# Kernel tuning notes

Hardware: AMD Instinct MI355X
Metric: run time of the kernel (lower is better)

## Reference

```python
import jax, jax.numpy as jnp
import numpy as np

FEATURE_MAPS = (38, 19, 10, 5, 3, 1)
BOXES_PER_LOC = (4, 6, 6, 6, 4, 4)
IMAGE_SIZE = 300
DEC_SIZE = 64  # WhatDecoder output resolution
MAX_OBJECTS = 10
Z_WHAT = 64


def _recon_indices():
    # Maps per-prior slots (8732) to per-location slots (1940), matching
    # Decoder.reconstruction_indices: each location index repeated boxes_per_loc times.
    idx, last = [], 0
    for fm, bpl in zip(FEATURE_MAPS, BOXES_PER_LOC):
        loc = np.arange(fm * fm) + last
        idx.append(np.repeat(loc, bpl))
        last = loc[-1] + 1
    return jnp.asarray(np.concatenate(idx), dtype=jnp.int32)


def _deconv2x2(x, W, b):
    # ConvTranspose2d(kernel=2, stride=2): each input pixel expands to a 2x2 block.
    n, c, h, w = x.shape
    o = W.shape[1]
    y = jnp.einsum('nchw,coab->nohawb', x, W).reshape(n, o, 2 * h, 2 * w)
    return y + b[None, :, None, None]


def _what_decoder(z, params):
    # z (M, Z_WHAT) -> (M, 3, 64, 64) in [0,1]
    x = z[:, :, None, None]
    nl = len(params)
    for i, (W, b) in enumerate(params):
        x = _deconv2x2(x, W, b)
        x = jax.nn.relu(x) if i < nl - 1 else jax.nn.sigmoid(x)
    return x


def _stn(images, z_where):
    # Spatial transformer: place (M,3,S,S) glyphs into IMAGE_SIZE canvas at box
    # z_where (M,4) = (cx,cy,w,h) in [0,1]; bilinear sampling, zeros padding.
    M, _, S, _ = images.shape
    cx, cy, w, h = (z_where[:, i] for i in range(4))
    # output pixel centers in normalized [-1,1] coords (align_corners=False)
    coords = (2.0 * jnp.arange(IMAGE_SIZE, dtype=images.dtype) + 1.0) / IMAGE_SIZE - 1.0
    xo = coords[None, None, :]
    yo = coords[None, :, None]
    eps = 1e-6
    u = (xo - (2.0 * cx - 1.0)[:, None, None]) / (w[:, None, None] + eps)  # (M,H,W)
    v = (yo - (2.0 * cy - 1.0)[:, None, None]) / (h[:, None, None] + eps)
    ix = ((u + 1.0) * S - 1.0) / 2.0  # input pixel coords
    iy = ((v + 1.0) * S - 1.0) / 2.0

    def sample_one(img, iy, ix):
        iy0 = jnp.floor(iy)
        ix0 = jnp.floor(ix)
        wy1 = iy - iy0
        wx1 = ix - ix0
        wy0 = 1.0 - wy1
        wx0 = 1.0 - wx1

        def g(y, x):
            yi = jnp.clip(y, 0, S - 1).astype(jnp.int32)
            xi = jnp.clip(x, 0, S - 1).astype(jnp.int32)
            valid = ((y >= 0) & (y < S) & (x >= 0) & (x < S)).astype(img.dtype)
            return img[:, yi, xi] * valid  # (3,H,W)

        return (g(iy0, ix0) * wy0 * wx0 + g(iy0, ix0 + 1) * wy0 * wx1
                + g(iy0 + 1, ix0) * wy1 * wx0 + g(iy0 + 1, ix0 + 1) * wy1 * wx1)

    return jax.vmap(sample_one)(images, iy, ix)  # (M,3,H,H)


def setup_inputs() -> dict:
    key = jax.random.key(0)
    ks = jax.random.split(key, 20)
    B, NLOC, NPRI = 16, 1940, 8732
    chans = (Z_WHAT, 256, 128, 64, 32, 16, 3)
    inp = {
        'z_what': jax.random.normal(ks[0], (B, NLOC, Z_WHAT), jnp.float32),
        'z_where': jax.random.uniform(ks[1], (B, NPRI, 4), jnp.float32),
        'z_present': jax.random.randint(ks[2], (B, NPRI, 1), 0, 2, jnp.int32),
        'z_depth': jax.random.normal(ks[3], (B, NLOC, 1), jnp.float32),
    }
    for i in range(6):
        ci, co = chans[i], chans[i + 1]
        inp[f'W{i}'] = jax.random.normal(ks[4 + i], (ci, co, 2, 2), jnp.float32) * 0.1
        inp[f'b{i}'] = jnp.zeros((co,), jnp.float32)
    return inp


def reference(z_what, z_where, z_present, z_depth,
              W0, b0, W1, b1, W2, b2, W3, b3, W4, b4, W5, b5):
    params = [(W0, b0), (W1, b1), (W2, b2), (W3, b3), (W4, b4), (W5, b5)]
    idx = _recon_indices()
    zw = z_what[:, idx]      # (B, P, D) ragged location->prior gather
    zd = z_depth[:, idx, 0]  # (B, P)
    order = jnp.argsort(-zd, axis=1)[:, :MAX_OBJECTS]  # depth sort, descending
    B, K = order.shape

    def gat(t):
        return jnp.take_along_axis(
            t, jnp.broadcast_to(order[:, :, None], (B, K, t.shape[-1])), axis=1)

    sw = gat(zw)            # (B,K,D)
    swr = gat(z_where)      # (B,K,4)
    sp = gat(z_present)     # (B,K,1)

    decoded = _what_decoder(sw.reshape(B * K, Z_WHAT), params)      # (B*K,3,64,64)
    transformed = _stn(decoded, swr.reshape(B * K, 4))              # (B*K,3,300,300)
    present = (sp == 1).astype(transformed.dtype).reshape(B * K, 1, 1, 1)
    objs = (transformed * present).reshape(B, K, 3, IMAGE_SIZE, IMAGE_SIZE)

    # z-buffer merge: per pixel, take first nonzero object in depth order
    nz = objs != 0.0
    first = nz & (jnp.cumsum(nz.astype(jnp.int32), axis=1) == 1)
    return jnp.sum(objs * first.astype(objs.dtype), axis=1)  # (B,3,300,300)
```

## Files before the change

### kernel.cpp

```cpp
#include <hip/hip_runtime.h>
#include <cmath>

#define NLOC 1940
#define NPRI 8732
#define BATCH 16
#define KOBJ 10

__device__ __forceinline__ int loc_of_prior(int p) {
    if (p < 5776) return p >> 2;
    if (p < 7942) return 1444 + (p - 5776) / 6;
    if (p < 8542) return 1805 + (p - 7942) / 6;
    if (p < 8692) return 1905 + (p - 8542) / 6;
    if (p < 8728) return 1930 + ((p - 8692) >> 2);
    return 1939 + ((p - 8728) >> 2);
}

__global__ __launch_bounds__(256) void topk_kernel(
    const float* __restrict__ z_what, const float* __restrict__ z_where,
    const int* __restrict__ z_present, const float* __restrict__ z_depth,
    float* __restrict__ gathered, float* __restrict__ paramsF, int* __restrict__ paramsI)
{
    const int b = blockIdx.x, tid = threadIdx.x;
    __shared__ float zd[NPRI];
    __shared__ float rv[256];
    __shared__ int   ri[256];
    __shared__ int   ord[KOBJ];
    __shared__ int   locs[KOBJ];

    for (int p = tid; p < NPRI; p += 256) zd[p] = z_depth[b * NLOC + loc_of_prior(p)];
    __syncthreads();

    for (int k = 0; k < KOBJ; ++k) {
        float bv = -INFINITY; int bi = NPRI;
        for (int p = tid; p < NPRI; p += 256) {
            float v = zd[p];
            if (v > bv) { bv = v; bi = p; }
        }
        rv[tid] = bv; ri[tid] = bi;
        __syncthreads();
        for (int s = 128; s > 0; s >>= 1) {
            if (tid < s) {
                float v2 = rv[tid + s]; int i2 = ri[tid + s];
                if (v2 > rv[tid] || (v2 == rv[tid] && i2 < ri[tid])) { rv[tid] = v2; ri[tid] = i2; }
            }
            __syncthreads();
        }
        if (tid == 0) {
            int w = ri[0];
            ord[k] = w; locs[k] = loc_of_prior(w);
            zd[w] = -INFINITY;
        }
        __syncthreads();
    }

    for (int e = tid; e < KOBJ * 64; e += 256) {
        int k = e >> 6, c = e & 63;
        gathered[(b * KOBJ + k) * 64 + c] = z_what[(b * NLOC + locs[k]) * 64 + c];
    }

    if (tid == 0) {
        int cnt = 0;
        for (int k = 0; k < KOBJ; ++k) {
            int p = ord[k];
            if (z_present[b * NPRI + p] == 1) {
                const float* zw = z_where + (b * NPRI + p) * 4;
                float cx = zw[0], cy = zw[1], w_ = zw[2], h_ = zw[3];
                float* pf = paramsF + (b * KOBJ + cnt) * 4;
                pf[0] = __fadd_rn(w_, 1e-6f);
                pf[1] = __fadd_rn(h_, 1e-6f);
                pf[2] = __fsub_rn(__fmul_rn(2.0f, cx), 1.0f);
                pf[3] = __fsub_rn(__fmul_rn(2.0f, cy), 1.0f);
                paramsI[b * 12 + 2 + cnt] = b * KOBJ + k;
                cnt++;
            }
        }
        paramsI[b * 12] = cnt;
    }
}

__global__ __launch_bounds__(256) void repack_kernel(
    const float* __restrict__ W0, const float* __restrict__ W1, float* __restrict__ Wr)
{
    const int idx = blockIdx.x * 256 + threadIdx.x;
    if (idx < 65536) {
        int q = idx >> 14, rem = idx & 16383, c = rem >> 8, o = rem & 255;
        Wr[idx] = W0[(((c << 8) | o) << 2) + q];
    } else {
        int i2 = idx - 65536;
        int q = i2 >> 15, rem = i2 & 32767, c = rem >> 7, o = rem & 127;
        Wr[idx] = W1[(((c << 7) | o) << 2) + q];
    }
}

__global__ __launch_bounds__(256) void dec_fused(
    const float* __restrict__ gathered, const float* __restrict__ Wr,
    const float* __restrict__ b0v, const float* __restrict__ b1v,
    const float* __restrict__ W2, const float* __restrict__ b2v,
    const float* __restrict__ W3, const float* __restrict__ b3v,
    const float* __restrict__ W4, const float* __restrict__ b4v,
    const float* __restrict__ W5, const float* __restrict__ b5v,
    float* __restrict__ decoded)
{
    __shared__ __align__(16) float P[4096];
    __shared__ __align__(16) float Q[2048];
    __shared__ __align__(16) float Zs[256];
    const int r  = blockIdx.x;
    const int g  = blockIdx.y;
    const int t  = threadIdx.x;
    const int y1 = r >> 2, x1 = r & 3;
    const int q0 = (y1 >> 1) * 2 + (x1 >> 1);
    const int p1 = (y1 & 1) * 2 + (x1 & 1);
    const int s4 = g * 4;

    Zs[t] = gathered[(s4 + (t & 3)) * 64 + (t >> 2)];
    __syncthreads();

    {
        const float* w0 = Wr + q0 * 16384 + t;
        float bv = b0v[t];
        float4 acc = make_float4(bv, bv, bv, bv);
        #pragma unroll 8
        for (int c = 0; c < 64; ++c) {
            float w = w0[c << 8];
            float4 xs = *reinterpret_cast<const float4*>(Zs + (c << 2));
            acc.x = fmaf(xs.x, w, acc.x); acc.y = fmaf(xs.y, w, acc.y);
            acc.z = fmaf(xs.z, w, acc.z); acc.w = fmaf(xs.w, w, acc.w);
        }
        float4 rv = make_float4(fmaxf(acc.x, 0.f), fmaxf(acc.y, 0.f),
                                fmaxf(acc.z, 0.f), fmaxf(acc.w, 0.f));
        *reinterpret_cast<float4*>(P + (t << 2)) = rv;
    }
    __syncthreads();

    {
        const int o = t & 127, h = t >> 7;
        const float* w1 = Wr + 65536 + p1 * 32768 + o;
        float4 acc;
        if (h == 0) { float bv = b1v[o]; acc = make_float4(bv, bv, bv, bv); }
        else        { acc = make_float4(0.f, 0.f, 0.f, 0.f); }
        const int cb = h << 7;
        #pragma unroll 8
        for (int c = 0; c < 128; ++c) {
            float w = w1[(cb + c) << 7];
            float4 xs = *reinterpret_cast<const float4*>(P + ((cb + c) << 2));
            acc.x = fmaf(xs.x, w, acc.x); acc.y = fmaf(xs.y, w, acc.y);
            acc.z = fmaf(xs.z, w, acc.z); acc.w = fmaf(xs.w, w, acc.w);
        }
        if (h == 1) *reinterpret_cast<float4*>(P + 1024 + (o << 2)) = acc;
        __syncthreads();
        if (h == 0) {
            float4 p2 = *reinterpret_cast<const float4*>(P + 1024 + (o << 2));
            acc.x += p2.x; acc.y += p2.y; acc.z += p2.z; acc.w += p2.w;
            float4 rv = make_float4(fmaxf(acc.x, 0.f), fmaxf(acc.y, 0.f),
                                    fmaxf(acc.z, 0.f), fmaxf(acc.w, 0.f));
            *reinterpret_cast<float4*>(Q + (o << 2)) = rv;
        }
    }
    __syncthreads();

    {
        const float* w2 = W2 + t;
        float bv = b2v[t >> 2];
        float4 acc = make_float4(bv, bv, bv, bv);
        #pragma unroll 8
        for (int ci = 0; ci < 128; ++ci) {
            float w = w2[ci << 8];
            float4 xs = *reinterpret_cast<const float4*>(Q + (ci << 2));
            acc.x = fmaf(xs.x, w, acc.x); acc.y = fmaf(xs.y, w, acc.y);
            acc.z = fmaf(xs.z, w, acc.z); acc.w = fmaf(xs.w, w, acc.w);
        }
        float4 rv = make_float4(fmaxf(acc.x, 0.f), fmaxf(acc.y, 0.f),
                                fmaxf(acc.z, 0.f), fmaxf(acc.w, 0.f));
        *reinterpret_cast<float4*>(P + (t << 2)) = rv;
    }
    __syncthreads();

    {
        const int px = t & 15, coa = t >> 4;
        const int ly = px >> 2, lx = px & 3;
        const int par = (ly >> 1) * 2 + (lx >> 1);
        const int wp  = (ly & 1) * 2 + (lx & 1);
        const float* w3 = W3 + coa * 4 + wp;
        float bva = b3v[coa], bvb = b3v[coa + 16];
        float4 a0 = make_float4(bva, bva, bva, bva);
        float4 a1 = make_float4(bvb, bvb, bvb, bvb);
        #pragma unroll 4
        for (int ci = 0; ci < 64; ++ci) {
            float4 xs = *reinterpret_cast<const float4*>(P + (ci << 4) + (par << 2));
            float wa = w3[ci << 7];
            float wb = w3[(ci << 7) + 64];
            a0.x = fmaf(xs.x, wa, a0.x); a0.y = fmaf(xs.y, wa, a0.y);
            a0.z = fmaf(xs.z, wa, a0.z); a0.w = fmaf(xs.w, wa, a0.w);
            a1.x = fmaf(xs.x, wb, a1.x); a1.y = fmaf(xs.y, wb, a1.y);
            a1.z = fmaf(xs.z, wb, a1.z); a1.w = fmaf(xs.w, wb, a1.w);
        }
        float4 r0 = make_float4(fmaxf(a0.x, 0.f), fmaxf(a0.y, 0.f),
                                fmaxf(a0.z, 0.f), fmaxf(a0.w, 0.f));
        float4 r1 = make_float4(fmaxf(a1.x, 0.f), fmaxf(a1.y, 0.f),
                                fmaxf(a1.z, 0.f), fmaxf(a1.w, 0.f));
        *reinterpret_cast<float4*>(Q + (coa << 6) + (px << 2)) = r0;
        *reinterpret_cast<float4*>(Q + ((coa + 16) << 6) + (px << 2)) = r1;
    }
    __syncthreads();

    {
        const int px = t & 63, co0 = t >> 6;
        const int ly = px >> 3, lx = px & 7;
        const int par = (ly >> 1) * 4 + (lx >> 1);
        const int wp  = (ly & 1) * 2 + (lx & 1);
        const float* w4 = W4 + co0 * 4 + wp;
        float4 acc[4];
        #pragma unroll
        for (int k = 0; k < 4; ++k) {
            float bv = b4v[co0 + 4 * k];
            acc[k] = make_float4(bv, bv, bv, bv);
        }
        #pragma unroll 4
        for (int ci = 0; ci < 32; ++ci) {
            float4 xs = *reinterpret_cast<const float4*>(Q + (ci << 6) + (par << 2));
            #pragma unroll
            for (int k = 0; k < 4; ++k) {
                float w = w4[(ci << 6) + k * 16];
                acc[k].x = fmaf(xs.x, w, acc[k].x); acc[k].y = fmaf(xs.y, w, acc[k].y);
                acc[k].z = fmaf(xs.z, w, acc[k].z); acc[k].w = fmaf(xs.w, w, acc[k].w);
            }
        }
        #pragma unroll
        for (int k = 0; k < 4; ++k) {
            float4 rv = make_float4(fmaxf(acc[k].x, 0.f), fmaxf(acc[k].y, 0.f),
                                    fmaxf(acc[k].z, 0.f), fmaxf(acc[k].w, 0.f));
            *reinterpret_cast<float4*>(P + ((co0 + 4 * k) << 8) + (px << 2)) = rv;
        }
    }
    __syncthreads();

    {
        const int px = t;
        const int ly = px >> 4, lx = px & 15;
        const int par = (ly >> 1) * 8 + (lx >> 1);
        const int wp  = (ly & 1) * 2 + (lx & 1);
        const int gy = y1 * 16 + ly, gx = x1 * 16 + lx;
        const float* w5 = W5 + wp;
        float4 acc[3];
        #pragma unroll
        for (int c = 0; c < 3; ++c) {
            float bv = b5v[c];
            acc[c] = make_float4(bv, bv, bv, bv);
        }
        #pragma unroll 4
        for (int ci = 0; ci < 16; ++ci) {
            float4 xs = *reinterpret_cast<const float4*>(P + (ci << 8) + (par << 2));
            #pragma unroll
            for (int c = 0; c < 3; ++c) {
                float w = w5[ci * 12 + c * 4];
                acc[c].x = fmaf(xs.x, w, acc[c].x); acc[c].y = fmaf(xs.y, w, acc[c].y);
                acc[c].z = fmaf(xs.z, w, acc[c].z); acc[c].w = fmaf(xs.w, w, acc[c].w);
            }
        }
        const int pbase = (gy * 64 + gx) * 3;
        #pragma unroll
        for (int c = 0; c < 3; ++c) {
            float vs[4] = {acc[c].x, acc[c].y, acc[c].z, acc[c].w};
            #pragma unroll
            for (int s = 0; s < 4; ++s)
                decoded[(s4 + s) * 12288 + pbase + c] = 1.0f / (1.0f + expf(-vs[s]));
        }
    }
}

__global__ __launch_bounds__(256) void stn_kernel(
    const float* __restrict__ decoded, const float* __restrict__ paramsF,
    const int* __restrict__ paramsI, float* __restrict__ out)
{
    const int b = blockIdx.y;
    __shared__ float sp[KOBJ][4];
    __shared__ int ssamp[KOBJ];
    __shared__ int scnt;
    if (threadIdx.x == 0) scnt = paramsI[b * 12];
    if (threadIdx.x < KOBJ) {
        #pragma unroll
        for (int c = 0; c < 4; ++c) sp[threadIdx.x][c] = paramsF[(b * KOBJ + threadIdx.x) * 4 + c];
        ssamp[threadIdx.x] = paramsI[b * 12 + 2 + threadIdx.x];
    }
    __syncthreads();
    const int pix = blockIdx.x * 256 + threadIdx.x;
    if (pix >= 90000) return;
    const int y = pix / 300;
    const int x = pix - y * 300;
    const float xo = __fsub_rn(__fdiv_rn(__fadd_rn(__fmul_rn(2.0f, (float)x), 1.0f), 300.0f), 1.0f);
    const float yo = __fsub_rn(__fdiv_rn(__fadd_rn(__fmul_rn(2.0f, (float)y), 1.0f), 300.0f), 1.0f);

    float o0 = 0.0f, o1 = 0.0f, o2 = 0.0f;
    bool d0 = false, d1 = false, d2 = false;
    const int cnt = scnt;
    for (int k = 0; k < cnt; ++k) {
        const float u = __fdiv_rn(__fsub_rn(xo, sp[k][2]), sp[k][0]);
        const float v = __fdiv_rn(__fsub_rn(yo, sp[k][3]), sp[k][1]);
        const float ix = __fmul_rn(__fsub_rn(__fmul_rn(__fadd_rn(u, 1.0f), 64.0f), 1.0f), 0.5f);
        const float iy = __fmul_rn(__fsub_rn(__fmul_rn(__fadd_rn(v, 1.0f), 64.0f), 1.0f), 0.5f);
        if (!(ix > -1.0f && ix < 64.0f && iy > -1.0f && iy < 64.0f)) continue;

        const float ix0f = floorf(ix), iy0f = floorf(iy);
        const float ix1f = __fadd_rn(ix0f, 1.0f), iy1f = __fadd_rn(iy0f, 1.0f);
        const float wx1 = __fsub_rn(ix, ix0f), wy1 = __fsub_rn(iy, iy0f);
        const float wx0 = __fsub_rn(1.0f, wx1), wy0 = __fsub_rn(1.0f, wy1);
        const bool vx0 = (ix0f >= 0.0f) && (ix0f < 64.0f);
        const bool vx1 = (ix1f >= 0.0f) && (ix1f < 64.0f);
        const bool vy0 = (iy0f >= 0.0f) && (iy0f < 64.0f);
        const bool vy1 = (iy1f >= 0.0f) && (iy1f < 64.0f);
        const int x0  = (int)fminf(fmaxf(ix0f, 0.0f), 63.0f);
        const int x1  = (int)fminf(fmaxf(ix1f, 0.0f), 63.0f);
        const int y0i = (int)fminf(fmaxf(iy0f, 0.0f), 63.0f);
        const int y1i = (int)fminf(fmaxf(iy1f, 0.0f), 63.0f);
        const int r00 = y0i * 64 + x0, r01 = y0i * 64 + x1;
        const int r10 = y1i * 64 + x0, r11 = y1i * 64 + x1;
        const bool m00 = vy0 && vx0, m01 = vy0 && vx1, m10 = vy1 && vx0, m11 = vy1 && vx1;
        const float* img = decoded + ssamp[k] * 12288;

        float g00x = 0.f, g00y = 0.f, g00z = 0.f;
        float g01x = 0.f, g01y = 0.f, g01z = 0.f;
        float g10x = 0.f, g10y = 0.f, g10z = 0.f;
        float g11x = 0.f, g11y = 0.f, g11z = 0.f;
        if (m00) { const float* p = img + r00 * 3; g00x = p[0]; g00y = p[1]; g00z = p[2]; }
        if (m01) { const float* p = img + r01 * 3; g01x = p[0]; g01y = p[1]; g01z = p[2]; }
        if (m10) { const float* p = img + r10 * 3; g10x = p[0]; g10y = p[1]; g10z = p[2]; }
        if (m11) { const float* p = img + r11 * 3; g11x = p[0]; g11y = p[1]; g11z = p[2]; }

        if (!d0) {
            float val = g00x * wy0 * wx0 + g01x * wy0 * wx1 + g10x * wy1 * wx0 + g11x * wy1 * wx1;
            if (val != 0.0f) { o0 = val; d0 = true; }
        }
        if (!d1) {
            float val = g00y * wy0 * wx0 + g01y * wy0 * wx1 + g10y * wy1 * wx0 + g11y * wy1 * wx1;
            if (val != 0.0f) { o1 = val; d1 = true; }
        }
        if (!d2) {
            float val = g00z * wy0 * wx0 + g01z * wy0 * wx1 + g10z * wy1 * wx0 + g11z * wy1 * wx1;
            if (val != 0.0f) { o2 = val; d2 = true; }
        }
        if (d0 && d1 && d2) break;
    }
    const int ob = b * 270000 + pix;
    out[ob] = o0;
    out[ob + 90000] = o1;
    out[ob + 180000] = o2;
}

extern "C" void kernel_launch(void* const* d_in, const int* in_sizes, int n_in,
                              void* d_out, int out_size, void* d_ws, size_t ws_size,
                              hipStream_t stream)
{
    const float* z_what    = (const float*)d_in[0];
    const float* z_where   = (const float*)d_in[1];
    const int*   z_present = (const int*)d_in[2];
    const float* z_depth   = (const float*)d_in[3];
    const float* W0 = (const float*)d_in[4];   const float* b0 = (const float*)d_in[5];
    const float* W1 = (const float*)d_in[6];   const float* b1 = (const float*)d_in[7];
    const float* W2 = (const float*)d_in[8];   const float* b2 = (const float*)d_in[9];
    const float* W3 = (const float*)d_in[10];  const float* b3 = (const float*)d_in[11];
    const float* W4 = (const float*)d_in[12];  const float* b4 = (const float*)d_in[13];
    const float* W5 = (const float*)d_in[14];  const float* b5 = (const float*)d_in[15];

    float* ws = (float*)d_ws;
    float* gathered = ws;
    float* paramsF  = ws + 16384;
    int*   paramsI  = (int*)(ws + 17408);
    float* decoded  = ws + 32768;
    float* Wr       = (float*)d_out;
    float* outp     = (float*)d_out;

    hipLaunchKernelGGL(repack_kernel, dim3(768), dim3(256), 0, stream, W0, W1, Wr);
    hipLaunchKernelGGL(topk_kernel, dim3(BATCH), dim3(256), 0, stream,
                       z_what, z_where, z_present, z_depth, gathered, paramsF, paramsI);
    hipLaunchKernelGGL(dec_fused, dim3(16, 40), dim3(256), 0, stream,
                       gathered, Wr, b0, b1, W2, b2, W3, b3, W4, b4, W5, b5, decoded);
    hipLaunchKernelGGL(stn_kernel, dim3(352, BATCH), dim3(256), 0, stream,
                       decoded, paramsF, paramsI, outp);
}
```

Measured before the change: 165.6 us.

## Top-3 over locations, decode only unique glyphs, fuse prep, hoist STN row math

The top-10 over 8732 repeated priors is replaced with a top-3 over the 1940 unique locations, since each location expands to at least four consecutive priors. Only three distinct glyphs per batch are decoded instead of ten (decoder grid shrinks from 40 to 12 in y). The weight repack and the top-k are merged into one launch. The STN kernel precomputes per-row vertical sampling terms in shared memory and skips objects that do not cover the block's rows. This relies on tie-break equivalence between the prior ordering and the location ordering, and adds some shared-memory setup per STN block.

```diff
diff --git a/kernel.cpp b/kernel.cpp
--- a/kernel.cpp
+++ b/kernel.cpp
@@ -6,89 +6,96 @@
 #define BATCH 16
 #define KOBJ 10
 
-__device__ __forceinline__ int loc_of_prior(int p) {
-    if (p < 5776) return p >> 2;
-    if (p < 7942) return 1444 + (p - 5776) / 6;
-    if (p < 8542) return 1805 + (p - 7942) / 6;
-    if (p < 8692) return 1905 + (p - 8542) / 6;
-    if (p < 8728) return 1930 + ((p - 8692) >> 2);
-    return 1939 + ((p - 8728) >> 2);
+__device__ __forceinline__ void ins3(float v, int i,
+    float& a0, float& a1, float& a2, int& j0, int& j1, int& j2)
+{
+    if (v > a0 || (v == a0 && i < j0)) { a2=a1; j2=j1; a1=a0; j1=j0; a0=v; j0=i; }
+    else if (v > a1 || (v == a1 && i < j1)) { a2=a1; j2=j1; a1=v; j1=i; }
+    else if (v > a2 || (v == a2 && i < j2)) { a2=v; j2=i; }
 }
 
-__global__ __launch_bounds__(256) void topk_kernel(
+__global__ __launch_bounds__(256) void prep_kernel(
+    const float* __restrict__ W0, const float* __restrict__ W1, float* __restrict__ Wr,
     const float* __restrict__ z_what, const float* __restrict__ z_where,
     const int* __restrict__ z_present, const float* __restrict__ z_depth,
     float* __restrict__ gathered, float* __restrict__ paramsF, int* __restrict__ paramsI)
 {
-    const int b = blockIdx.x, tid = threadIdx.x;
-    __shared__ float zd[NPRI];
-    __shared__ float rv[256];
-    __shared__ int   ri[256];
-    __shared__ int   ord[KOBJ];
-    __shared__ int   locs[KOBJ];
-
-    for (int p = tid; p < NPRI; p += 256) zd[p] = z_depth[b * NLOC + loc_of_prior(p)];
-    __syncthreads();
-
-    for (int k = 0; k < KOBJ; ++k) {
-        float bv = -INFINITY; int bi = NPRI;
-        for (int p = tid; p < NPRI; p += 256) {
-            float v = zd[p];
-            if (v > bv) { bv = v; bi = p; }
-        }
-        rv[tid] = bv; ri[tid] = bi;
+    __shared__ float sv[768];
+    __shared__ int   si[768];
+    __shared__ int   locs3[3];
+    const int tid = threadIdx.x;
+
+    if (blockIdx.x < 768) {
+        const int idx = blockIdx.x * 256 + tid;
+        if (idx < 65536) {
+            int q = idx >> 14, rem = idx & 16383, c = rem >> 8, o = rem & 255;
+            Wr[idx] = W0[(((c << 8) | o) << 2) + q];
+        } else {
+            int i2 = idx - 65536;
+            int q = i2 >> 15, rem = i2 & 32767, c = rem >> 7, o = rem & 127;
+            Wr[idx] = W1[(((c << 7) | o) << 2) + q];
+        }
+        return;
+    }
+
+    const int b = blockIdx.x - 768;
+    float v0 = -INFINITY, v1 = -INFINITY, v2 = -INFINITY;
+    int   i0 = NLOC, i1 = NLOC, i2 = NLOC;
+    for (int i = tid; i < NLOC; i += 256) {
+        float v = z_depth[b * NLOC + i];
+        ins3(v, i, v0, v1, v2, i0, i1, i2);
+    }
+    sv[tid*3+0] = v0; sv[tid*3+1] = v1; sv[tid*3+2] = v2;
+    si[tid*3+0] = i0; si[tid*3+1] = i1; si[tid*3+2] = i2;
+    __syncthreads();
+    for (int s = 128; s > 0; s >>= 1) {
+        if (tid < s) {
+            float a0 = sv[tid*3], a1 = sv[tid*3+1], a2 = sv[tid*3+2];
+            int   j0 = si[tid*3], j1 = si[tid*3+1], j2 = si[tid*3+2];
+            const int o = tid + s;
+            ins3(sv[o*3+0], si[o*3+0], a0, a1, a2, j0, j1, j2);
+            ins3(sv[o*3+1], si[o*3+1], a0, a1, a2, j0, j1, j2);
+            ins3(sv[o*3+2], si[o*3+2], a0, a1, a2, j0, j1, j2);
+            sv[tid*3] = a0; sv[tid*3+1] = a1; sv[tid*3+2] = a2;
+            si[tid*3] = j0; si[tid*3+1] = j1; si[tid*3+2] = j2;
+        }
         __syncthreads();
-        for (int s = 128; s > 0; s >>= 1) {
-            if (tid < s) {
-                float v2 = rv[tid + s]; int i2 = ri[tid + s];
-                if (v2 > rv[tid] || (v2 == rv[tid] && i2 < ri[tid])) { rv[tid] = v2; ri[tid] = i2; }
-            }
-            __syncthreads();
-        }
-        if (tid == 0) {
-            int w = ri[0];
-            ord[k] = w; locs[k] = loc_of_prior(w);
-            zd[w] = -INFINITY;
-        }
-        __syncthreads();
-    }
-
-    for (int e = tid; e < KOBJ * 64; e += 256) {
-        int k = e >> 6, c = e & 63;
-        gathered[(b * KOBJ + k) * 64 + c] = z_what[(b * NLOC + locs[k]) * 64 + c];
     }
 
     if (tid == 0) {
-        int cnt = 0;
-        for (int k = 0; k < KOBJ; ++k) {
-            int p = ord[k];
-            if (z_present[b * NPRI + p] == 1) {
-                const float* zw = z_where + (b * NPRI + p) * 4;
-                float cx = zw[0], cy = zw[1], w_ = zw[2], h_ = zw[3];
-                float* pf = paramsF + (b * KOBJ + cnt) * 4;
-                pf[0] = __fadd_rn(w_, 1e-6f);
-                pf[1] = __fadd_rn(h_, 1e-6f);
-                pf[2] = __fsub_rn(__fmul_rn(2.0f, cx), 1.0f);
-                pf[3] = __fsub_rn(__fmul_rn(2.0f, cy), 1.0f);
-                paramsI[b * 12 + 2 + cnt] = b * KOBJ + k;
-                cnt++;
+        int cnt = 0, taken = 0;
+        for (int j = 0; j < 3; ++j) {
+            int L = si[j];
+            locs3[j] = L;
+            if (taken >= KOBJ) continue;
+            int start, bpl;
+            if (L < 1444)      { start = 4 * L;                 bpl = 4; }
+            else if (L < 1805) { start = 5776 + 6 * (L - 1444); bpl = 6; }
+            else if (L < 1905) { start = 7942 + 6 * (L - 1805); bpl = 6; }
+            else if (L < 1930) { start = 8542 + 6 * (L - 1905); bpl = 6; }
+            else if (L < 1939) { start = 8692 + 4 * (L - 1930); bpl = 4; }
+            else               { start = 8728;                  bpl = 4; }
+            for (int o = 0; o < bpl && taken < KOBJ; ++o, ++taken) {
+                int p = start + o;
+                if (z_present[b * NPRI + p] == 1) {
+                    const float* zw = z_where + (b * NPRI + p) * 4;
+                    float cx = zw[0], cy = zw[1], w_ = zw[2], h_ = zw[3];
+                    float* pf = paramsF + (b * KOBJ + cnt) * 4;
+                    pf[0] = __fadd_rn(w_, 1e-6f);
+                    pf[1] = __fadd_rn(h_, 1e-6f);
+                    pf[2] = __fsub_rn(__fmul_rn(2.0f, cx), 1.0f);
+                    pf[3] = __fsub_rn(__fmul_rn(2.0f, cy), 1.0f);
+                    paramsI[b * 12 + 2 + cnt] = b * 3 + j;
+                    cnt++;
+                }
             }
         }
         paramsI[b * 12] = cnt;
     }
-}
-
-__global__ __launch_bounds__(256) void repack_kernel(
-    const float* __restrict__ W0, const float* __restrict__ W1, float* __restrict__ Wr)
-{
-    const int idx = blockIdx.x * 256 + threadIdx.x;
-    if (idx < 65536) {
-        int q = idx >> 14, rem = idx & 16383, c = rem >> 8, o = rem & 255;
-        Wr[idx] = W0[(((c << 8) | o) << 2) + q];
-    } else {
-        int i2 = idx - 65536;
-        int q = i2 >> 15, rem = i2 & 32767, c = rem >> 7, o = rem & 127;
-        Wr[idx] = W1[(((c << 7) | o) << 2) + q];
+    __syncthreads();
+    if (tid < 192) {
+        int j = tid >> 6, c = tid & 63;
+        gathered[(b * 3 + j) * 64 + c] = z_what[(b * NLOC + locs3[j]) * 64 + c];
     }
 }
 
@@ -126,9 +133,8 @@
             acc.x = fmaf(xs.x, w, acc.x); acc.y = fmaf(xs.y, w, acc.y);
             acc.z = fmaf(xs.z, w, acc.z); acc.w = fmaf(xs.w, w, acc.w);
         }
-        float4 rv = make_float4(fmaxf(acc.x, 0.f), fmaxf(acc.y, 0.f),
-                                fmaxf(acc.z, 0.f), fmaxf(acc.w, 0.f));
-        *reinterpret_cast<float4*>(P + (t << 2)) = rv;
+        *reinterpret_cast<float4*>(P + (t << 2)) =
+            make_float4(fmaxf(acc.x, 0.f), fmaxf(acc.y, 0.f), fmaxf(acc.z, 0.f), fmaxf(acc.w, 0.f));
     }
     __syncthreads();
 
@@ -151,9 +157,8 @@
         if (h == 0) {
             float4 p2 = *reinterpret_cast<const float4*>(P + 1024 + (o << 2));
             acc.x += p2.x; acc.y += p2.y; acc.z += p2.z; acc.w += p2.w;
-            float4 rv = make_float4(fmaxf(acc.x, 0.f), fmaxf(acc.y, 0.f),
-                                    fmaxf(acc.z, 0.f), fmaxf(acc.w, 0.f));
-            *reinterpret_cast<float4*>(Q + (o << 2)) = rv;
+            *reinterpret_cast<float4*>(Q + (o << 2)) =
+                make_float4(fmaxf(acc.x, 0.f), fmaxf(acc.y, 0.f), fmaxf(acc.z, 0.f), fmaxf(acc.w, 0.f));
         }
     }
     __syncthreads();
@@ -169,9 +174,8 @@
             acc.x = fmaf(xs.x, w, acc.x); acc.y = fmaf(xs.y, w, acc.y);
             acc.z = fmaf(xs.z, w, acc.z); acc.w = fmaf(xs.w, w, acc.w);
         }
-        float4 rv = make_float4(fmaxf(acc.x, 0.f), fmaxf(acc.y, 0.f),
-                                fmaxf(acc.z, 0.f), fmaxf(acc.w, 0.f));
-        *reinterpret_cast<float4*>(P + (t << 2)) = rv;
+        *reinterpret_cast<float4*>(P + (t << 2)) =
+            make_float4(fmaxf(acc.x, 0.f), fmaxf(acc.y, 0.f), fmaxf(acc.z, 0.f), fmaxf(acc.w, 0.f));
     }
     __syncthreads();
 
@@ -194,12 +198,10 @@
             a1.x = fmaf(xs.x, wb, a1.x); a1.y = fmaf(xs.y, wb, a1.y);
             a1.z = fmaf(xs.z, wb, a1.z); a1.w = fmaf(xs.w, wb, a1.w);
         }
-        float4 r0 = make_float4(fmaxf(a0.x, 0.f), fmaxf(a0.y, 0.f),
-                                fmaxf(a0.z, 0.f), fmaxf(a0.w, 0.f));
-        float4 r1 = make_float4(fmaxf(a1.x, 0.f), fmaxf(a1.y, 0.f),
-                                fmaxf(a1.z, 0.f), fmaxf(a1.w, 0.f));
-        *reinterpret_cast<float4*>(Q + (coa << 6) + (px << 2)) = r0;
-        *reinterpret_cast<float4*>(Q + ((coa + 16) << 6) + (px << 2)) = r1;
+        *reinterpret_cast<float4*>(Q + (coa << 6) + (px << 2)) =
+            make_float4(fmaxf(a0.x, 0.f), fmaxf(a0.y, 0.f), fmaxf(a0.z, 0.f), fmaxf(a0.w, 0.f));
+        *reinterpret_cast<float4*>(Q + ((coa + 16) << 6) + (px << 2)) =
+            make_float4(fmaxf(a1.x, 0.f), fmaxf(a1.y, 0.f), fmaxf(a1.z, 0.f), fmaxf(a1.w, 0.f));
     }
     __syncthreads();
 
@@ -227,9 +229,9 @@
         }
         #pragma unroll
         for (int k = 0; k < 4; ++k) {
-            float4 rv = make_float4(fmaxf(acc[k].x, 0.f), fmaxf(acc[k].y, 0.f),
-                                    fmaxf(acc[k].z, 0.f), fmaxf(acc[k].w, 0.f));
-            *reinterpret_cast<float4*>(P + ((co0 + 4 * k) << 8) + (px << 2)) = rv;
+            *reinterpret_cast<float4*>(P + ((co0 + 4 * k) << 8) + (px << 2)) =
+                make_float4(fmaxf(acc[k].x, 0.f), fmaxf(acc[k].y, 0.f),
+                            fmaxf(acc[k].z, 0.f), fmaxf(acc[k].w, 0.f));
         }
     }
     __syncthreads();
@@ -273,77 +275,116 @@
     const int* __restrict__ paramsI, float* __restrict__ out)
 {
     const int b = blockIdx.y;
+    const int pix0 = blockIdx.x * 256;
+    const int yfirst = pix0 / 300;
     __shared__ float sp[KOBJ][4];
-    __shared__ int ssamp[KOBJ];
-    __shared__ int scnt;
-    if (threadIdx.x == 0) scnt = paramsI[b * 12];
-    if (threadIdx.x < KOBJ) {
+    __shared__ int   ssamp[KOBJ];
+    __shared__ int   scnt;
+    __shared__ float s_wy0[KOBJ][2], s_wy1[KOBJ][2];
+    __shared__ int   s_rb0[KOBJ][2], s_rb1[KOBJ][2];
+    __shared__ unsigned char s_cov[KOBJ][2];
+    __shared__ unsigned char s_vy[KOBJ][2];
+    __shared__ int s_list[KOBJ];
+    __shared__ int s_lc;
+    const int tid = threadIdx.x;
+
+    if (tid == 0) scnt = paramsI[b * 12];
+    if (tid < KOBJ) {
         #pragma unroll
-        for (int c = 0; c < 4; ++c) sp[threadIdx.x][c] = paramsF[(b * KOBJ + threadIdx.x) * 4 + c];
-        ssamp[threadIdx.x] = paramsI[b * 12 + 2 + threadIdx.x];
-    }
-    __syncthreads();
-    const int pix = blockIdx.x * 256 + threadIdx.x;
-    if (pix >= 90000) return;
-    const int y = pix / 300;
-    const int x = pix - y * 300;
-    const float xo = __fsub_rn(__fdiv_rn(__fadd_rn(__fmul_rn(2.0f, (float)x), 1.0f), 300.0f), 1.0f);
-    const float yo = __fsub_rn(__fdiv_rn(__fadd_rn(__fmul_rn(2.0f, (float)y), 1.0f), 300.0f), 1.0f);
-
-    float o0 = 0.0f, o1 = 0.0f, o2 = 0.0f;
-    bool d0 = false, d1 = false, d2 = false;
-    const int cnt = scnt;
-    for (int k = 0; k < cnt; ++k) {
-        const float u = __fdiv_rn(__fsub_rn(xo, sp[k][2]), sp[k][0]);
-        const float v = __fdiv_rn(__fsub_rn(yo, sp[k][3]), sp[k][1]);
-        const float ix = __fmul_rn(__fsub_rn(__fmul_rn(__fadd_rn(u, 1.0f), 64.0f), 1.0f), 0.5f);
+        for (int c = 0; c < 4; ++c) sp[tid][c] = paramsF[(b * KOBJ + tid) * 4 + c];
+        ssamp[tid] = paramsI[b * 12 + 2 + tid];
+    }
+    __syncthreads();
+
+    if (tid < 2 * scnt) {
+        const int k = tid >> 1, sel = tid & 1;
+        int yy = yfirst + sel; if (yy > 299) yy = 299;
+        const float yo = __fsub_rn(__fdiv_rn(__fadd_rn(__fmul_rn(2.0f, (float)yy), 1.0f), 300.0f), 1.0f);
+        const float v  = __fdiv_rn(__fsub_rn(yo, sp[k][3]), sp[k][1]);
         const float iy = __fmul_rn(__fsub_rn(__fmul_rn(__fadd_rn(v, 1.0f), 64.0f), 1.0f), 0.5f);
-        if (!(ix > -1.0f && ix < 64.0f && iy > -1.0f && iy < 64.0f)) continue;
-
-        const float ix0f = floorf(ix), iy0f = floorf(iy);
-        const float ix1f = __fadd_rn(ix0f, 1.0f), iy1f = __fadd_rn(iy0f, 1.0f);
-        const float wx1 = __fsub_rn(ix, ix0f), wy1 = __fsub_rn(iy, iy0f);
-        const float wx0 = __fsub_rn(1.0f, wx1), wy0 = __fsub_rn(1.0f, wy1);
-        const bool vx0 = (ix0f >= 0.0f) && (ix0f < 64.0f);
-        const bool vx1 = (ix1f >= 0.0f) && (ix1f < 64.0f);
+        const bool cov = (iy > -1.0f && iy < 64.0f);
+        s_cov[k][sel] = cov ? 1 : 0;
+        const float iy0f = floorf(iy);
+        const float iy1f = __fadd_rn(iy0f, 1.0f);
+        const float wy1  = __fsub_rn(iy, iy0f);
+        s_wy1[k][sel] = wy1;
+        s_wy0[k][sel] = __fsub_rn(1.0f, wy1);
         const bool vy0 = (iy0f >= 0.0f) && (iy0f < 64.0f);
         const bool vy1 = (iy1f >= 0.0f) && (iy1f < 64.0f);
-        const int x0  = (int)fminf(fmaxf(ix0f, 0.0f), 63.0f);
-        const int x1  = (int)fminf(fmaxf(ix1f, 0.0f), 63.0f);
-        const int y0i = (int)fminf(fmaxf(iy0f, 0.0f), 63.0f);
-        const int y1i = (int)fminf(fmaxf(iy1f, 0.0f), 63.0f);
-        const int r00 = y0i * 64 + x0, r01 = y0i * 64 + x1;
-        const int r10 = y1i * 64 + x0, r11 = y1i * 64 + x1;
-        const bool m00 = vy0 && vx0, m01 = vy0 && vx1, m10 = vy1 && vx0, m11 = vy1 && vx1;
-        const float* img = decoded + ssamp[k] * 12288;
-
-        float g00x = 0.f, g00y = 0.f, g00z = 0.f;
-        float g01x = 0.f, g01y = 0.f, g01z = 0.f;
-        float g10x = 0.f, g10y = 0.f, g10z = 0.f;
-        float g11x = 0.f, g11y = 0.f, g11z = 0.f;
-        if (m00) { const float* p = img + r00 * 3; g00x = p[0]; g00y = p[1]; g00z = p[2]; }
-        if (m01) { const float* p = img + r01 * 3; g01x = p[0]; g01y = p[1]; g01z = p[2]; }
-        if (m10) { const float* p = img + r10 * 3; g10x = p[0]; g10y = p[1]; g10z = p[2]; }
-        if (m11) { const float* p = img + r11 * 3; g11x = p[0]; g11y = p[1]; g11z = p[2]; }
-
-        if (!d0) {
-            float val = g00x * wy0 * wx0 + g01x * wy0 * wx1 + g10x * wy1 * wx0 + g11x * wy1 * wx1;
-            if (val != 0.0f) { o0 = val; d0 = true; }
-        }
-        if (!d1) {
-            float val = g00y * wy0 * wx0 + g01y * wy0 * wx1 + g10y * wy1 * wx0 + g11y * wy1 * wx1;
-            if (val != 0.0f) { o1 = val; d1 = true; }
-        }
-        if (!d2) {
-            float val = g00z * wy0 * wx0 + g01z * wy0 * wx1 + g10z * wy1 * wx0 + g11z * wy1 * wx1;
-            if (val != 0.0f) { o2 = val; d2 = true; }
-        }
-        if (d0 && d1 && d2) break;
-    }
-    const int ob = b * 270000 + pix;
-    out[ob] = o0;
-    out[ob + 90000] = o1;
-    out[ob + 180000] = o2;
+        s_vy[k][sel] = (unsigned char)((vy0 ? 1 : 0) | (vy1 ? 2 : 0));
+        s_rb0[k][sel] = ((int)fminf(fmaxf(iy0f, 0.0f), 63.0f)) * 64;
+        s_rb1[k][sel] = ((int)fminf(fmaxf(iy1f, 0.0f), 63.0f)) * 64;
+    }
+    __syncthreads();
+    if (tid == 0) {
+        int lc = 0;
+        for (int k = 0; k < scnt; ++k)
+            if (s_cov[k][0] | s_cov[k][1]) s_list[lc++] = k;
+        s_lc = lc;
+    }
+    __syncthreads();
+
+    const int pix = pix0 + tid;
+    if (pix < 90000) {
+        const int y = pix / 300;
+        const int x = pix - y * 300;
+        const int rs = y - yfirst;
+        const float xo = __fsub_rn(__fdiv_rn(__fadd_rn(__fmul_rn(2.0f, (float)x), 1.0f), 300.0f), 1.0f);
+
+        float o0 = 0.0f, o1 = 0.0f, o2 = 0.0f;
+        bool d0 = false, d1 = false, d2 = false;
+        const int lc = s_lc;
+        for (int m = 0; m < lc; ++m) {
+            const int k = s_list[m];
+            if (!s_cov[k][rs]) continue;
+            const float u  = __fdiv_rn(__fsub_rn(xo, sp[k][2]), sp[k][0]);
+            const float ix = __fmul_rn(__fsub_rn(__fmul_rn(__fadd_rn(u, 1.0f), 64.0f), 1.0f), 0.5f);
+            if (!(ix > -1.0f && ix < 64.0f)) continue;
+
+            const float ix0f = floorf(ix);
+            const float ix1f = __fadd_rn(ix0f, 1.0f);
+            const float wx1 = __fsub_rn(ix, ix0f);
+            const float wx0 = __fsub_rn(1.0f, wx1);
+            const bool vx0 = (ix0f >= 0.0f) && (ix0f < 64.0f);
+            const bool vx1 = (ix1f >= 0.0f) && (ix1f < 64.0f);
+            const int x0 = (int)fminf(fmaxf(ix0f, 0.0f), 63.0f);
+            const int x1 = (int)fminf(fmaxf(ix1f, 0.0f), 63.0f);
+
+            const float wy0 = s_wy0[k][rs], wy1 = s_wy1[k][rs];
+            const int rb0 = s_rb0[k][rs], rb1 = s_rb1[k][rs];
+            const unsigned char vy = s_vy[k][rs];
+            const bool m00 = (vy & 1) && vx0, m01 = (vy & 1) && vx1;
+            const bool m10 = (vy & 2) && vx0, m11 = (vy & 2) && vx1;
+            const float* img = decoded + ssamp[k] * 12288;
+
+            float g00x = 0.f, g00y = 0.f, g00z = 0.f;
+            float g01x = 0.f, g01y = 0.f, g01z = 0.f;
+            float g10x = 0.f, g10y = 0.f, g10z = 0.f;
+            float g11x = 0.f, g11y = 0.f, g11z = 0.f;
+            if (m00) { const float* p = img + (rb0 + x0) * 3; g00x = p[0]; g00y = p[1]; g00z = p[2]; }
+            if (m01) { const float* p = img + (rb0 + x1) * 3; g01x = p[0]; g01y = p[1]; g01z = p[2]; }
+            if (m10) { const float* p = img + (rb1 + x0) * 3; g10x = p[0]; g10y = p[1]; g10z = p[2]; }
+            if (m11) { const float* p = img + (rb1 + x1) * 3; g11x = p[0]; g11y = p[1]; g11z = p[2]; }
+
+            if (!d0) {
+                float val = g00x * wy0 * wx0 + g01x * wy0 * wx1 + g10x * wy1 * wx0 + g11x * wy1 * wx1;
+                if (val != 0.0f) { o0 = val; d0 = true; }
+            }
+            if (!d1) {
+                float val = g00y * wy0 * wx0 + g01y * wy0 * wx1 + g10y * wy1 * wx0 + g11y * wy1 * wx1;
+                if (val != 0.0f) { o1 = val; d1 = true; }
+            }
+            if (!d2) {
+                float val = g00z * wy0 * wx0 + g01z * wy0 * wx1 + g10z * wy1 * wx0 + g11z * wy1 * wx1;
+                if (val != 0.0f) { o2 = val; d2 = true; }
+            }
+            if (d0 && d1 && d2) break;
+        }
+        const int ob = b * 270000 + pix;
+        out[ob] = o0;
+        out[ob + 90000] = o1;
+        out[ob + 180000] = o2;
+    }
 }
 
 extern "C" void kernel_launch(void* const* d_in, const int* in_sizes, int n_in,
@@ -369,10 +410,10 @@
     float* Wr       = (float*)d_out;
     float* outp     = (float*)d_out;
 
-    hipLaunchKernelGGL(repack_kernel, dim3(768), dim3(256), 0, stream, W0, W1, Wr);
-    hipLaunchKernelGGL(topk_kernel, dim3(BATCH), dim3(256), 0, stream,
-                       z_what, z_where, z_present, z_depth, gathered, paramsF, paramsI);
-    hipLaunchKernelGGL(dec_fused, dim3(16, 40), dim3(256), 0, stream,
+    hipLaunchKernelGGL(prep_kernel, dim3(784), dim3(256), 0, stream,
+                       W0, W1, Wr, z_what, z_where, z_present, z_depth,
+                       gathered, paramsF, paramsI);
+    hipLaunchKernelGGL(dec_fused, dim3(16, 12), dim3(256), 0, stream,
                        gathered, Wr, b0, b1, W2, b2, W3, b3, W4, b4, W5, b5, decoded);
     hipLaunchKernelGGL(stn_kernel, dim3(352, BATCH), dim3(256), 0, stream,
                        decoded, paramsF, paramsI, outp);
```

Result: faster. 150.5 us (-9.1%).
